# Optimization experiments

Hardware: AMD Instinct MI355X
Metric: run time of the kernel (lower is better)

## Reference

```python
import jax, jax.numpy as jnp
import numpy as np

K = 7          # kernel_size
PAD = 3        # padding = (K - 1) // 2, stride = 1
H, W = 2048, 2048


def _design_pinv():
    # Same design matrix as the torch module: plane z = C0*x + C1*y + C2
    half = (K - 1) / 2
    space = np.arange(-half, half + 1, 1)
    X, Y = np.meshgrid(space, space)              # 'xy' indexing, matches np.meshgrid default
    A = np.c_[X.flatten(), Y.flatten(), np.ones(K * K)].astype(np.float32)  # [K*K, 3]
    # lstsq with full-column-rank A == pinv(A) @ v
    return jnp.asarray(np.linalg.pinv(A).astype(np.float32))  # [3, K*K]


def setup_inputs() -> dict:
    key = jax.random.key(0)
    x = jax.random.normal(key, (H, W), dtype=jnp.float32)
    return {"x": x}


def reference(x):
    h, w = x.shape
    # ReplicationPad2d == edge padding
    xp = jnp.pad(x, PAD, mode='edge')[None, None]  # [1, 1, h+2P, w+2P]
    # Extract all KxK patches; with 1 input channel the K*K channel dim is
    # kernel-row-major, matching unfold(2,K,1).unfold(3,K,1).view(N, K*K).
    patches = jax.lax.conv_general_dilated_patches(
        xp, (K, K), (1, 1), 'VALID')               # [1, K*K, h, w]
    pv = patches.reshape(K * K, h * w).T            # [h*w, K*K]
    pinvA = _design_pinv()                          # [3, K*K]
    cs = pv @ pinvA.T                               # [h*w, 3] plane coeffs per pixel
    return cs.reshape(h, w, 3)
```

## Files before the change

### kernel.cpp

```cpp
#include <hip/hip_runtime.h>

#define HH 2048
#define WW 2048
#define KK 7
#define PADK 3
#define TILE 32
#define PADT (TILE + 6)
#define IN_STRIDE (PADT + 2)
#define HS_STRIDE (TILE + 1)

__global__ __launch_bounds__(256)
void UnfoldPlainFit_42477226558039_kernel(const float* __restrict__ x,
                                          float* __restrict__ out) {
    __shared__ float sIn[PADT][IN_STRIDE];
    __shared__ float sHs[PADT][HS_STRIDE];
    __shared__ float sHx[PADT][HS_STRIDE];

    const int tileR = blockIdx.y * TILE;
    const int tileC = blockIdx.x * TILE;
    const int tid = threadIdx.x;

    for (int idx = tid; idx < PADT * PADT; idx += 256) {
        int lr = idx / PADT;
        int lc = idx - lr * PADT;
        int gr = tileR - PADK + lr;
        int gc = tileC - PADK + lc;
        gr = max(0, min(HH - 1, gr));
        gc = max(0, min(WW - 1, gc));
        sIn[lr][lc] = x[(size_t)gr * WW + gc];
    }
    __syncthreads();

    for (int idx = tid; idx < PADT * TILE; idx += 256) {
        int lr = idx >> 5;
        int oc = idx & 31;
        float s = 0.f, wx = 0.f;
#pragma unroll
        for (int j = 0; j < KK; ++j) {
            float v = sIn[lr][oc + j];
            s += v;
            wx += (float)(j - PADK) * v;
        }
        sHs[lr][oc] = s;
        sHx[lr][oc] = wx;
    }
    __syncthreads();

    const int row = tid >> 3;
    const int cg  = (tid & 7) * 4;

    float c0[4] = {0.f, 0.f, 0.f, 0.f};
    float c1[4] = {0.f, 0.f, 0.f, 0.f};
    float c2[4] = {0.f, 0.f, 0.f, 0.f};
#pragma unroll
    for (int i = 0; i < KK; ++i) {
        float wy = (float)(i - PADK);
#pragma unroll
        for (int u = 0; u < 4; ++u) {
            float hs = sHs[row + i][cg + u];
            float hx = sHx[row + i][cg + u];
            c2[u] += hs;
            c1[u] += wy * hs;
            c0[u] += hx;
        }
    }
    const float W196 = 1.0f / 196.0f;
    const float W49  = 1.0f / 49.0f;

    int r = tileR + row;
    int c = tileC + cg;
    float* o = out + ((size_t)r * WW + c) * 3;
    float4 v0 = {c0[0] * W196, c1[0] * W196, c2[0] * W49,  c0[1] * W196};
    float4 v1 = {c1[1] * W196, c2[1] * W49,  c0[2] * W196, c1[2] * W196};
    float4 v2 = {c2[2] * W49,  c0[3] * W196, c1[3] * W196, c2[3] * W49};
    float4* o4 = reinterpret_cast<float4*>(o);
    o4[0] = v0;
    o4[1] = v1;
    o4[2] = v2;
}

extern "C" void kernel_launch(void* const* d_in, const int* in_sizes, int n_in,
                              void* d_out, int out_size, void* d_ws, size_t ws_size,
                              hipStream_t stream) {
    const float* x = (const float*)d_in[0];
    float* out = (float*)d_out;
    dim3 grid(WW / TILE, HH / TILE);
    dim3 block(256);
    UnfoldPlainFit_42477226558039_kernel<<<grid, block, 0, stream>>>(x, out);
}
```

Measured before the change: 93.73 us.

## Vectorize tile loads, LDS passes, and use nontemporal output stores

Interior tiles now load the halo region with aligned float4 global reads into a 40-wide shared buffer, and only edge tiles fall back to clamped scalar loads. The horizontal pass has each thread compute four outputs from three float4 LDS reads. The vertical pass reads float4s from shared memory, and output stores use nontemporal hints. The aim is to cut load and LDS instruction counts and avoid cache pollution from the write-heavy output, at the cost of a branchy load path and shared-memory layouts without padding that may cause bank conflicts.

```diff
diff --git a/kernel.cpp b/kernel.cpp
--- a/kernel.cpp
+++ b/kernel.cpp
@@ -5,78 +5,100 @@
 #define KK 7
 #define PADK 3
 #define TILE 32
-#define PADT (TILE + 6)
-#define IN_STRIDE (PADT + 2)
-#define HS_STRIDE (TILE + 1)
+#define PADT 38
+#define INW 40
+#define INW4 (INW / 4)
+#define HSW 36
+#define HSW4 (HSW / 4)
+
+typedef float v4f __attribute__((ext_vector_type(4)));
 
 __global__ __launch_bounds__(256)
 void UnfoldPlainFit_42477226558039_kernel(const float* __restrict__ x,
                                           float* __restrict__ out) {
-    __shared__ float sIn[PADT][IN_STRIDE];
-    __shared__ float sHs[PADT][HS_STRIDE];
-    __shared__ float sHx[PADT][HS_STRIDE];
+    __shared__ float sIn[PADT][INW];
+    __shared__ float sHs[PADT][HSW];
+    __shared__ float sHx[PADT][HSW];
 
-    const int tileR = blockIdx.y * TILE;
-    const int tileC = blockIdx.x * TILE;
+    const int bx = blockIdx.x, by = blockIdx.y;
+    const int tileR = by * TILE, tileC = bx * TILE;
     const int tid = threadIdx.x;
 
-    for (int idx = tid; idx < PADT * PADT; idx += 256) {
-        int lr = idx / PADT;
-        int lc = idx - lr * PADT;
-        int gr = tileR - PADK + lr;
-        int gc = tileC - PADK + lc;
-        gr = max(0, min(HH - 1, gr));
-        gc = max(0, min(WW - 1, gc));
-        sIn[lr][lc] = x[(size_t)gr * WW + gc];
+    if (bx > 0 && bx < (WW / TILE - 1)) {
+#pragma unroll 2
+        for (int idx = tid; idx < PADT * INW4; idx += 256) {
+            int lr = idx / INW4;
+            int k  = idx - lr * INW4;
+            int gr = tileR - PADK + lr;
+            gr = max(0, min(HH - 1, gr));
+            const v4f* src =
+                reinterpret_cast<const v4f*>(x + (size_t)gr * WW + (tileC - 4)) + k;
+            reinterpret_cast<v4f*>(&sIn[lr][0])[k] = *src;
+        }
+    } else {
+        for (int idx = tid; idx < PADT * INW; idx += 256) {
+            int lr = idx / INW;
+            int lc = idx - lr * INW;
+            int gr = max(0, min(HH - 1, tileR - PADK + lr));
+            int gc = max(0, min(WW - 1, tileC - 4 + lc));
+            sIn[lr][lc] = x[(size_t)gr * WW + gc];
+        }
     }
     __syncthreads();
 
-    for (int idx = tid; idx < PADT * TILE; idx += 256) {
-        int lr = idx >> 5;
-        int oc = idx & 31;
-        float s = 0.f, wx = 0.f;
+#pragma unroll 2
+    for (int idx = tid; idx < PADT * 8; idx += 256) {
+        int lr = idx >> 3;
+        int u  = idx & 7;
+        const v4f* row4 = reinterpret_cast<const v4f*>(&sIn[lr][0]);
+        v4f a = row4[u], b = row4[u + 1], c = row4[u + 2];
+        float w[12] = {a.x, a.y, a.z, a.w, b.x, b.y, b.z, b.w, c.x, c.y, c.z, c.w};
+        v4f hs, hx;
 #pragma unroll
-        for (int j = 0; j < KK; ++j) {
-            float v = sIn[lr][oc + j];
-            s += v;
-            wx += (float)(j - PADK) * v;
+        for (int t = 0; t < 4; ++t) {
+            float s = 0.f, wx = 0.f;
+#pragma unroll
+            for (int m = 0; m < KK; ++m) {
+                float v = w[1 + t + m];
+                s += v;
+                wx = fmaf((float)(m - PADK), v, wx);
+            }
+            hs[t] = s;
+            hx[t] = wx;
         }
-        sHs[lr][oc] = s;
-        sHx[lr][oc] = wx;
+        reinterpret_cast<v4f*>(&sHs[lr][0])[u] = hs;
+        reinterpret_cast<v4f*>(&sHx[lr][0])[u] = hx;
     }
     __syncthreads();
 
     const int row = tid >> 3;
-    const int cg  = (tid & 7) * 4;
-
+    const int u   = tid & 7;
     float c0[4] = {0.f, 0.f, 0.f, 0.f};
     float c1[4] = {0.f, 0.f, 0.f, 0.f};
     float c2[4] = {0.f, 0.f, 0.f, 0.f};
 #pragma unroll
     for (int i = 0; i < KK; ++i) {
+        v4f hs = reinterpret_cast<const v4f*>(&sHs[row + i][0])[u];
+        v4f hx = reinterpret_cast<const v4f*>(&sHx[row + i][0])[u];
         float wy = (float)(i - PADK);
 #pragma unroll
-        for (int u = 0; u < 4; ++u) {
-            float hs = sHs[row + i][cg + u];
-            float hx = sHx[row + i][cg + u];
-            c2[u] += hs;
-            c1[u] += wy * hs;
-            c0[u] += hx;
+        for (int t = 0; t < 4; ++t) {
+            c2[t] += hs[t];
+            c1[t] = fmaf(wy, hs[t], c1[t]);
+            c0[t] += hx[t];
         }
     }
     const float W196 = 1.0f / 196.0f;
     const float W49  = 1.0f / 49.0f;
 
-    int r = tileR + row;
-    int c = tileC + cg;
-    float* o = out + ((size_t)r * WW + c) * 3;
-    float4 v0 = {c0[0] * W196, c1[0] * W196, c2[0] * W49,  c0[1] * W196};
-    float4 v1 = {c1[1] * W196, c2[1] * W49,  c0[2] * W196, c1[2] * W196};
-    float4 v2 = {c2[2] * W49,  c0[3] * W196, c1[3] * W196, c2[3] * W49};
-    float4* o4 = reinterpret_cast<float4*>(o);
-    o4[0] = v0;
-    o4[1] = v1;
-    o4[2] = v2;
+    float* o = out + ((size_t)(tileR + row) * WW + tileC + 4 * u) * 3;
+    v4f v0 = {c0[0] * W196, c1[0] * W196, c2[0] * W49,  c0[1] * W196};
+    v4f v1 = {c1[1] * W196, c2[1] * W49,  c0[2] * W196, c1[2] * W196};
+    v4f v2 = {c2[2] * W49,  c0[3] * W196, c1[3] * W196, c2[3] * W49};
+    v4f* o4 = reinterpret_cast<v4f*>(o);
+    __builtin_nontemporal_store(v0, o4 + 0);
+    __builtin_nontemporal_store(v1, o4 + 1);
+    __builtin_nontemporal_store(v2, o4 + 2);
 }
 
 extern "C" void kernel_launch(void* const* d_in, const int* in_sizes, int n_in,
```

Measured after the change: 98.80 us. 5.4% more time.
